# Performance work log

Hardware: AMD Instinct MI355X
Metric: run time of the kernel (lower is better)

Reference implementation:

```python
import jax, jax.numpy as jnp
import numpy as np

B, T, FC, FX = 64, 1024, 256, 512

def setup_inputs() -> dict:
    key = jax.random.key(0)
    kC, kX, kW, kb = jax.random.split(key, 4)
    C = jax.random.normal(kC, (B, T, FC), dtype=jnp.float32)
    X = jax.random.normal(kX, (B, T, FX), dtype=jnp.float32)
    # nn.Linear(encoding_size, context_size): W [fc, fx], b [fc]
    lim = 1.0 / np.sqrt(FX)
    W = jax.random.uniform(kW, (FC, FX), minval=-lim, maxval=lim, dtype=jnp.float32)
    b = jax.random.uniform(kb, (FC,), minval=-lim, maxval=lim, dtype=jnp.float32)
    return {"C": C, "X": X, "W": W, "b": b}

def reference(C, X, W, b):
    # Xt = Linear(X): [B, T, fc]
    Xt = jnp.einsum('btx,cx->btc', X, W) + b
    # Z[i, j, t] = <C[i, t, :], Xt[j, t, :]>  -> per-timestep BxB similarity
    Z = jnp.einsum('itc,jtc->ijt', C, Xt)
    # logsumexp over the negatives axis (dim 1), numerically stable
    lse = jax.nn.logsumexp(Z, axis=1)          # [B, T]
    Zdiag = jnp.einsum('iit->it', Z)           # [B, T], Z[i, i, t]
    return jnp.mean(Zdiag - lse)
```

## Files before the change

### kernel.cpp

```cpp
#include <hip/hip_runtime.h>

#define B_  64
#define T_  1024
#define FC_ 256
#define FX_ 512

typedef __bf16 bf16x8 __attribute__((ext_vector_type(8)));
typedef float  f32x4  __attribute__((ext_vector_type(4)));

__device__ __forceinline__ unsigned short f2bf(float f) {
  union { float f; unsigned int u; } v; v.f = f;
  unsigned int r = v.u + 0x7fffu + ((v.u >> 16) & 1u);
  return (unsigned short)(r >> 16);
}
__device__ __forceinline__ unsigned int pk2(float lo, float hi) {
  return (unsigned int)f2bf(lo) | ((unsigned int)f2bf(hi) << 16);
}
__device__ __forceinline__ uint4 pk8(float4 a, float4 b) {
  uint4 p;
  p.x = pk2(a.x, a.y); p.y = pk2(a.z, a.w);
  p.z = pk2(b.x, b.y); p.w = pk2(b.z, b.w);
  return p;
}

__global__ void k_wcvt(const float* __restrict__ W, unsigned short* __restrict__ Wb,
                       float* __restrict__ out) {
  const int i = blockIdx.x * 256 + threadIdx.x;
  float4 v = ((const float4*)W)[i];
  ushort4 h;
  h.x = f2bf(v.x); h.y = f2bf(v.y); h.z = f2bf(v.z); h.w = f2bf(v.w);
  ((ushort4*)Wb)[i] = h;
  if (i == 0) out[0] = 0.f;
}

__global__ __launch_bounds__(512, 4)
void k_fused(const float* __restrict__ C, const float* __restrict__ X,
             const unsigned short* __restrict__ Wb, const float* __restrict__ bias,
             float* __restrict__ out)
{
  __shared__ __align__(16) char sMem[65536];
  char* sX  = sMem;
  char* sXt = sMem;

  const int t    = blockIdx.x;
  const int tid  = threadIdx.x;
  const int lane = tid & 63;
  const int wid  = tid >> 6;
  const int l15  = lane & 15;
  const int lhi  = lane >> 4;

  const int xrow = tid >> 3;
  const int xg   = tid & 7;
  const float* xptr = X + ((size_t)xrow * T_ + t) * FX_ + xg * 8;

  float4 xv[16];
  #pragma unroll
  for (int q = 0; q < 8; ++q) {
    xv[2 * q]     = *(const float4*)(xptr + 64 * q);
    xv[2 * q + 1] = *(const float4*)(xptr + 64 * q + 4);
  }

  const float bv0 = bias[wid * 32 + l15];
  const float bv1 = bias[wid * 32 + 16 + l15];

  f32x4 acc[4][2];
  #pragma unroll
  for (int i = 0; i < 4; ++i)
    #pragma unroll
    for (int n2 = 0; n2 < 2; ++n2)
      #pragma unroll
      for (int r = 0; r < 4; ++r) acc[i][n2][r] = 0.f;

  const int xswz = (xrow & 7) << 4;
  #pragma unroll
  for (int q = 0; q < 8; ++q) {
    *(uint4*)(sX + xrow * 1024 + ((xg * 16 + 128 * q) ^ xswz)) =
        pk8(xv[2 * q], xv[2 * q + 1]);
  }
  __syncthreads();

  const char* wrow = (const char*)Wb + (size_t)(wid * 32 + l15) * 1024 + lhi * 16;
  bf16x8 wc0 = *(const bf16x8*)(wrow);
  bf16x8 wc1 = *(const bf16x8*)(wrow + 16384);
  #pragma unroll
  for (int s = 0; s < 16; ++s) {
    bf16x8 wn0, wn1;
    if (s < 15) {
      wn0 = *(const bf16x8*)(wrow + (s + 1) * 64);
      wn1 = *(const bf16x8*)(wrow + 16384 + (s + 1) * 64);
    }
    bf16x8 afr[4];
    #pragma unroll
    for (int i = 0; i < 4; ++i) {
      const int ar = i * 16 + l15;
      afr[i] = *(const bf16x8*)(sX + ar * 1024 + ((s * 64 + lhi * 16) ^ ((ar & 7) << 4)));
    }
    #pragma unroll
    for (int i = 0; i < 4; ++i) {
      acc[i][0] = __builtin_amdgcn_mfma_f32_16x16x32_bf16(afr[i], wc0, acc[i][0], 0, 0, 0);
      acc[i][1] = __builtin_amdgcn_mfma_f32_16x16x32_bf16(afr[i], wc1, acc[i][1], 0, 0, 0);
    }
    if (s < 15) { wc0 = wn0; wc1 = wn1; }
  }
  __syncthreads();

  float4 cv[16];
  if (wid < 4) {
    const float* cptr = C + ((size_t)(wid * 16 + l15) * T_ + t) * FC_ + lhi * 8;
    #pragma unroll
    for (int s = 0; s < 8; ++s) {
      cv[2 * s]     = *(const float4*)(cptr + 32 * s);
      cv[2 * s + 1] = *(const float4*)(cptr + 32 * s + 4);
    }
  }

  {
    const int c0 = (wid * 32 + l15) * 2;
    const int c1 = (wid * 32 + 16 + l15) * 2;
    #pragma unroll
    for (int i = 0; i < 4; ++i)
      #pragma unroll
      for (int r = 0; r < 4; ++r) {
        const int j   = i * 16 + lhi * 4 + r;
        const int rsw = (j & 7) << 4;
        *(unsigned short*)(sXt + j * 512 + (c0 ^ rsw)) = f2bf(acc[i][0][r] + bv0);
        *(unsigned short*)(sXt + j * 512 + (c1 ^ rsw)) = f2bf(acc[i][1][r] + bv1);
      }
  }
  __syncthreads();

  if (wid < 4) {
    f32x4 z[4];
    #pragma unroll
    for (int n = 0; n < 4; ++n)
      #pragma unroll
      for (int r = 0; r < 4; ++r) z[n][r] = 0.f;

    #pragma unroll
    for (int s = 0; s < 8; ++s) {
      bf16x8 ca = __builtin_bit_cast(bf16x8, pk8(cv[2 * s], cv[2 * s + 1]));
      #pragma unroll
      for (int n = 0; n < 4; ++n) {
        const int br = n * 16 + l15;
        bf16x8 b = *(const bf16x8*)(sXt + br * 512 + ((s * 64 + lhi * 16) ^ ((br & 7) << 4)));
        z[n] = __builtin_amdgcn_mfma_f32_16x16x32_bf16(ca, b, z[n], 0, 0, 0);
      }
    }

    float partial = 0.f;
    #pragma unroll
    for (int r = 0; r < 4; ++r) {
      float m = fmaxf(fmaxf(z[0][r], z[1][r]), fmaxf(z[2][r], z[3][r]));
      #pragma unroll
      for (int d = 1; d < 16; d <<= 1) m = fmaxf(m, __shfl_xor(m, d));
      float s = __expf(z[0][r] - m) + __expf(z[1][r] - m) +
                __expf(z[2][r] - m) + __expf(z[3][r] - m);
      #pragma unroll
      for (int d = 1; d < 16; d <<= 1) s += __shfl_xor(s, d);
      const float lse = m + __logf(s);
      float dv = 0.f;
      #pragma unroll
      for (int n = 0; n < 4; ++n) dv = (n == wid) ? z[n][r] : dv;
      if (l15 == lhi * 4 + r) partial += dv - lse;
    }
    #pragma unroll
    for (int d = 1; d < 64; d <<= 1) partial += __shfl_xor(partial, d);
    if (lane == 0) atomicAdd(out, partial * (1.0f / (B_ * T_)));
  }
}

extern "C" void kernel_launch(void* const* d_in, const int* in_sizes, int n_in,
                              void* d_out, int out_size, void* d_ws, size_t ws_size,
                              hipStream_t stream) {
  const float* C  = (const float*)d_in[0];
  const float* X  = (const float*)d_in[1];
  const float* W  = (const float*)d_in[2];
  const float* bb = (const float*)d_in[3];
  unsigned short* Wb = (unsigned short*)d_ws;
  float* out = (float*)d_out;

  k_wcvt <<<dim3(128),  dim3(256), 0, stream>>>(W, Wb, out);
  k_fused<<<dim3(1024), dim3(512), 0, stream>>>(C, X, Wb, bb, out);
}
```

Baseline: 269.4 us.

## Split fused kernel into separate Xt GEMM and loss kernels via workspace

The single fused per-timestep kernel is split into two kernels. One computes Xt = X·Wᵀ + b as a flat GEMM over all B*T rows and writes bf16 results to a global workspace. A second kernel per timestep loads C and gathers Xt rows from global memory to compute the 64x64 logits and the logsumexp loss. This removes the shared-memory staging and the idle waves in the loss phase, and lets each kernel use its own tiling. The cost is an extra launch and a round trip of Xt through HBM (about 32 MB written and read). Loss-phase Xt reads are also strided across time.

```diff
diff --git a/kernel.cpp b/kernel.cpp
--- a/kernel.cpp
+++ b/kernel.cpp
@@ -16,15 +16,16 @@
 __device__ __forceinline__ unsigned int pk2(float lo, float hi) {
   return (unsigned int)f2bf(lo) | ((unsigned int)f2bf(hi) << 16);
 }
-__device__ __forceinline__ uint4 pk8(float4 a, float4 b) {
+__device__ __forceinline__ bf16x8 pk8(float4 a, float4 b) {
   uint4 p;
   p.x = pk2(a.x, a.y); p.y = pk2(a.z, a.w);
   p.z = pk2(b.x, b.y); p.w = pk2(b.z, b.w);
-  return p;
+  return __builtin_bit_cast(bf16x8, p);
 }
 
-__global__ void k_wcvt(const float* __restrict__ W, unsigned short* __restrict__ Wb,
-                       float* __restrict__ out) {
+__global__ __launch_bounds__(256)
+void k_wcvt(const float* __restrict__ W, unsigned short* __restrict__ Wb,
+            float* __restrict__ out) {
   const int i = blockIdx.x * 256 + threadIdx.x;
   float4 v = ((const float4*)W)[i];
   ushort4 h;
@@ -33,15 +34,58 @@
   if (i == 0) out[0] = 0.f;
 }
 
-__global__ __launch_bounds__(512, 4)
-void k_fused(const float* __restrict__ C, const float* __restrict__ X,
-             const unsigned short* __restrict__ Wb, const float* __restrict__ bias,
+__global__ __launch_bounds__(256, 4)
+void k1_xt(const float* __restrict__ X, const unsigned short* __restrict__ Wb,
+           const float* __restrict__ bias, unsigned short* __restrict__ Xt)
+{
+  const int tid  = threadIdx.x;
+  const int lane = tid & 63;
+  const int wid  = tid >> 6;
+  const int l15  = lane & 15;
+  const int lhi  = lane >> 4;
+  const int m0   = blockIdx.x * 64 + wid * 16;
+
+  const float* xrow  = X + (size_t)(m0 + l15) * FX_ + lhi * 8;
+  const char*  wbase = (const char*)Wb + (size_t)l15 * 1024 + lhi * 16;
+
+  f32x4 acc[16];
+  #pragma unroll
+  for (int n = 0; n < 16; ++n)
+    #pragma unroll
+    for (int r = 0; r < 4; ++r) acc[n][r] = 0.f;
+
+  #pragma unroll
+  for (int s = 0; s < 16; ++s) {
+    float4 a0 = *(const float4*)(xrow + s * 32);
+    float4 a1 = *(const float4*)(xrow + s * 32 + 4);
+    bf16x8 av = pk8(a0, a1);
+    #pragma unroll
+    for (int g = 0; g < 2; ++g) {
+      bf16x8 wv[8];
+      #pragma unroll
+      for (int j = 0; j < 8; ++j)
+        wv[j] = *(const bf16x8*)(wbase + (size_t)(g * 8 + j) * 16384 + s * 64);
+      #pragma unroll
+      for (int j = 0; j < 8; ++j)
+        acc[g * 8 + j] = __builtin_amdgcn_mfma_f32_16x16x32_bf16(av, wv[j], acc[g * 8 + j], 0, 0, 0);
+    }
+  }
+
+  #pragma unroll
+  for (int n = 0; n < 16; ++n) {
+    const float bb = bias[n * 16 + l15];
+    #pragma unroll
+    for (int r = 0; r < 4; ++r) {
+      const int m = m0 + lhi * 4 + r;
+      Xt[(size_t)m * FC_ + n * 16 + l15] = f2bf(acc[n][r] + bb);
+    }
+  }
+}
+
+__global__ __launch_bounds__(256, 4)
+void k2_loss(const float* __restrict__ C, const unsigned short* __restrict__ Xt,
              float* __restrict__ out)
 {
-  __shared__ __align__(16) char sMem[65536];
-  char* sX  = sMem;
-  char* sXt = sMem;
-
   const int t    = blockIdx.x;
   const int tid  = threadIdx.x;
   const int lane = tid & 63;
@@ -49,124 +93,51 @@
   const int l15  = lane & 15;
   const int lhi  = lane >> 4;
 
-  const int xrow = tid >> 3;
-  const int xg   = tid & 7;
-  const float* xptr = X + ((size_t)xrow * T_ + t) * FX_ + xg * 8;
-
-  float4 xv[16];
+  const float* cptr = C + ((size_t)(wid * 16 + l15) * T_ + t) * FC_ + lhi * 8;
+  float4 cv[16];
   #pragma unroll
   for (int q = 0; q < 8; ++q) {
-    xv[2 * q]     = *(const float4*)(xptr + 64 * q);
-    xv[2 * q + 1] = *(const float4*)(xptr + 64 * q + 4);
+    cv[2 * q]     = *(const float4*)(cptr + 32 * q);
+    cv[2 * q + 1] = *(const float4*)(cptr + 32 * q + 4);
   }
 
-  const float bv0 = bias[wid * 32 + l15];
-  const float bv1 = bias[wid * 32 + 16 + l15];
+  const char* xb = (const char*)Xt + (size_t)l15 * (T_ * FC_ * 2) + (size_t)t * (FC_ * 2) + lhi * 16;
 
-  f32x4 acc[4][2];
+  f32x4 z[4];
   #pragma unroll
-  for (int i = 0; i < 4; ++i)
+  for (int n = 0; n < 4; ++n)
     #pragma unroll
-    for (int n2 = 0; n2 < 2; ++n2)
-      #pragma unroll
-      for (int r = 0; r < 4; ++r) acc[i][n2][r] = 0.f;
+    for (int r = 0; r < 4; ++r) z[n][r] = 0.f;
 
-  const int xswz = (xrow & 7) << 4;
   #pragma unroll
-  for (int q = 0; q < 8; ++q) {
-    *(uint4*)(sX + xrow * 1024 + ((xg * 16 + 128 * q) ^ xswz)) =
-        pk8(xv[2 * q], xv[2 * q + 1]);
-  }
-  __syncthreads();
-
-  const char* wrow = (const char*)Wb + (size_t)(wid * 32 + l15) * 1024 + lhi * 16;
-  bf16x8 wc0 = *(const bf16x8*)(wrow);
-  bf16x8 wc1 = *(const bf16x8*)(wrow + 16384);
-  #pragma unroll
-  for (int s = 0; s < 16; ++s) {
-    bf16x8 wn0, wn1;
-    if (s < 15) {
-      wn0 = *(const bf16x8*)(wrow + (s + 1) * 64);
-      wn1 = *(const bf16x8*)(wrow + 16384 + (s + 1) * 64);
-    }
-    bf16x8 afr[4];
+  for (int s = 0; s < 8; ++s) {
+    bf16x8 ca = pk8(cv[2 * s], cv[2 * s + 1]);
     #pragma unroll
-    for (int i = 0; i < 4; ++i) {
-      const int ar = i * 16 + l15;
-      afr[i] = *(const bf16x8*)(sX + ar * 1024 + ((s * 64 + lhi * 16) ^ ((ar & 7) << 4)));
-    }
-    #pragma unroll
-    for (int i = 0; i < 4; ++i) {
-      acc[i][0] = __builtin_amdgcn_mfma_f32_16x16x32_bf16(afr[i], wc0, acc[i][0], 0, 0, 0);
-      acc[i][1] = __builtin_amdgcn_mfma_f32_16x16x32_bf16(afr[i], wc1, acc[i][1], 0, 0, 0);
-    }
-    if (s < 15) { wc0 = wn0; wc1 = wn1; }
-  }
-  __syncthreads();
-
-  float4 cv[16];
-  if (wid < 4) {
-    const float* cptr = C + ((size_t)(wid * 16 + l15) * T_ + t) * FC_ + lhi * 8;
-    #pragma unroll
-    for (int s = 0; s < 8; ++s) {
-      cv[2 * s]     = *(const float4*)(cptr + 32 * s);
-      cv[2 * s + 1] = *(const float4*)(cptr + 32 * s + 4);
+    for (int n = 0; n < 4; ++n) {
+      bf16x8 b = *(const bf16x8*)(xb + (size_t)n * 16 * (T_ * FC_ * 2) + s * 64);
+      z[n] = __builtin_amdgcn_mfma_f32_16x16x32_bf16(ca, b, z[n], 0, 0, 0);
     }
   }
 
-  {
-    const int c0 = (wid * 32 + l15) * 2;
-    const int c1 = (wid * 32 + 16 + l15) * 2;
+  float partial = 0.f;
+  #pragma unroll
+  for (int r = 0; r < 4; ++r) {
+    float m = fmaxf(fmaxf(z[0][r], z[1][r]), fmaxf(z[2][r], z[3][r]));
     #pragma unroll
-    for (int i = 0; i < 4; ++i)
-      #pragma unroll
-      for (int r = 0; r < 4; ++r) {
-        const int j   = i * 16 + lhi * 4 + r;
-        const int rsw = (j & 7) << 4;
-        *(unsigned short*)(sXt + j * 512 + (c0 ^ rsw)) = f2bf(acc[i][0][r] + bv0);
-        *(unsigned short*)(sXt + j * 512 + (c1 ^ rsw)) = f2bf(acc[i][1][r] + bv1);
-      }
+    for (int d = 1; d < 16; d <<= 1) m = fmaxf(m, __shfl_xor(m, d));
+    float s = __expf(z[0][r] - m) + __expf(z[1][r] - m) +
+              __expf(z[2][r] - m) + __expf(z[3][r] - m);
+    #pragma unroll
+    for (int d = 1; d < 16; d <<= 1) s += __shfl_xor(s, d);
+    const float lse = m + __logf(s);
+    float dv = 0.f;
+    #pragma unroll
+    for (int n = 0; n < 4; ++n) dv = (n == wid) ? z[n][r] : dv;
+    if (l15 == lhi * 4 + r) partial += dv - lse;
   }
-  __syncthreads();
-
-  if (wid < 4) {
-    f32x4 z[4];
-    #pragma unroll
-    for (int n = 0; n < 4; ++n)
-      #pragma unroll
-      for (int r = 0; r < 4; ++r) z[n][r] = 0.f;
-
-    #pragma unroll
-    for (int s = 0; s < 8; ++s) {
-      bf16x8 ca = __builtin_bit_cast(bf16x8, pk8(cv[2 * s], cv[2 * s + 1]));
-      #pragma unroll
-      for (int n = 0; n < 4; ++n) {
-        const int br = n * 16 + l15;
-        bf16x8 b = *(const bf16x8*)(sXt + br * 512 + ((s * 64 + lhi * 16) ^ ((br & 7) << 4)));
-        z[n] = __builtin_amdgcn_mfma_f32_16x16x32_bf16(ca, b, z[n], 0, 0, 0);
-      }
-    }
-
-    float partial = 0.f;
-    #pragma unroll
-    for (int r = 0; r < 4; ++r) {
-      float m = fmaxf(fmaxf(z[0][r], z[1][r]), fmaxf(z[2][r], z[3][r]));
-      #pragma unroll
-      for (int d = 1; d < 16; d <<= 1) m = fmaxf(m, __shfl_xor(m, d));
-      float s = __expf(z[0][r] - m) + __expf(z[1][r] - m) +
-                __expf(z[2][r] - m) + __expf(z[3][r] - m);
-      #pragma unroll
-      for (int d = 1; d < 16; d <<= 1) s += __shfl_xor(s, d);
-      const float lse = m + __logf(s);
-      float dv = 0.f;
-      #pragma unroll
-      for (int n = 0; n < 4; ++n) dv = (n == wid) ? z[n][r] : dv;
-      if (l15 == lhi * 4 + r) partial += dv - lse;
-    }
-    #pragma unroll
-    for (int d = 1; d < 64; d <<= 1) partial += __shfl_xor(partial, d);
-    if (lane == 0) atomicAdd(out, partial * (1.0f / (B_ * T_)));
-  }
+  #pragma unroll
+  for (int d = 1; d < 64; d <<= 1) partial += __shfl_xor(partial, d);
+  if (lane == 0) atomicAdd(out, partial * (1.0f / (B_ * T_)));
 }
 
 extern "C" void kernel_launch(void* const* d_in, const int* in_sizes, int n_in,
@@ -177,8 +148,10 @@
   const float* W  = (const float*)d_in[2];
   const float* bb = (const float*)d_in[3];
   unsigned short* Wb = (unsigned short*)d_ws;
+  unsigned short* Xt = (unsigned short*)d_ws + 131072;
   float* out = (float*)d_out;
 
   k_wcvt <<<dim3(128),  dim3(256), 0, stream>>>(W, Wb, out);
-  k_fused<<<dim3(1024), dim3(512), 0, stream>>>(C, X, Wb, bb, out);
+  k1_xt  <<<dim3(1024), dim3(256), 0, stream>>>(X, Wb, bb, Xt);
+  k2_loss<<<dim3(1024), dim3(256), 0, stream>>>(C, Xt, out);
 }
```

New measurement: 389.3 us. 44.5% more time.
